# Kernel optimization log

Hardware: AMD Instinct MI355X
Metric: run time of the kernel (lower is better)

The kernel has to match this reference:

```python
import jax, jax.numpy as jnp
import numpy as np

B = 16      # number of point clouds in the batch
N = 2048    # points per cloud
P = B * N   # total points (flat PyG-style batching)
K = 16      # neighbors per point (col 0 = self loop)
OUT = 512   # out_channels


def _linear(key, fi, fo):
    # torch nn.Linear default init: U(-1/sqrt(fi), 1/sqrt(fi))
    s = 1.0 / np.sqrt(fi)
    kw, kb = jax.random.split(key)
    W = jax.random.uniform(kw, (fi, fo), jnp.float32, -s, s)
    b = jax.random.uniform(kb, (fo,), jnp.float32, -s, s)
    return W, b


def setup_inputs() -> dict:
    key = jax.random.key(0)
    ks = jax.random.split(key, 6)
    pos = jax.random.normal(ks[0], (P, 3), jnp.float32)
    # flat batch vector: points are grouped contiguously per cloud
    batch = (jnp.arange(P, dtype=jnp.int32) // N).astype(jnp.int32)
    # within-cloud random neighbor indices (stand-in for knn/radius graph)
    base = (jnp.arange(P) // N) * N  # offset of each point's cloud
    nbr = base[:, None] + jax.random.randint(ks[1], (P, K), 0, N)
    nbr = nbr.at[:, 0].set(jnp.arange(P))  # self loop (PyG add_self_loops)
    W1, b1 = _linear(ks[2], 3, 64)          # sa1 MLP layer 1
    W2, b2 = _linear(ks[3], 64, 128)        # sa1 MLP layer 2
    W3, b3 = _linear(ks[4], 128 + 3, 256)   # sa2 MLP layer 1
    W4, b4 = _linear(ks[5], 256, OUT)       # sa2 MLP layer 2
    return dict(pos=pos, nbr=nbr.astype(jnp.int64), batch=batch,
                W1=W1, b1=b1, W2=W2, b2=b2, W3=W3, b3=b3, W4=W4, b4=b4)


def reference(pos, nbr, batch, W1, b1, W2, b2, W3, b3, W4, b4):
    # ----- sa1: x is None -> message = MLP(pos_j - pos_i), max-aggregated -----
    diff = pos[nbr] - pos[:, None, :]                      # [P, K, 3]
    h1 = jnp.maximum(diff @ W1 + b1, 0.0) @ W2 + b2        # [P, K, 128]
    x1 = jnp.max(h1, axis=1)                               # [P, 128]
    # ----- sa2: message = MLP([x1_j, pos_j - pos_i]), max-aggregated -----
    feats = jnp.concatenate([x1[nbr], diff], axis=-1)      # [P, K, 131]
    h2 = jnp.maximum(feats @ W3 + b3, 0.0) @ W4 + b4       # [P, K, 512]
    x2 = jnp.max(h2, axis=1)                               # [P, 512]
    # ----- global_max_pool over batch -----
    return jax.ops.segment_max(x2, batch, num_segments=B)  # [B, 512]
```

## Files before the change

kernel.cpp:

```cpp
#include <hip/hip_runtime.h>
#include <hip/hip_bf16.h>

#define PTOT   32768
#define KNB    16
#define NCLOUD 16
#define OUTC   512
#define A1S    168
#define A2S    264

typedef __attribute__((ext_vector_type(8)))  short v8bf;
typedef __attribute__((ext_vector_type(16))) float v16f;

__device__ __forceinline__ unsigned short f2b(float v) {
    __hip_bfloat16 h = __float2bfloat16(v);
    return *reinterpret_cast<unsigned short*>(&h);
}
__device__ __forceinline__ unsigned pk2(float a, float b) {
    return (unsigned)f2b(a) | ((unsigned)f2b(b) << 16);
}
__device__ __forceinline__ unsigned fenc(float f) {
    unsigned u = __float_as_uint(f);
    return (u & 0x80000000u) ? ~u : (u | 0x80000000u);
}
__device__ __forceinline__ float fdec(unsigned u) {
    unsigned b = (u & 0x80000000u) ? (u & 0x7FFFFFFFu) : ~u;
    return __uint_as_float(b);
}
__device__ __forceinline__ v16f zero16() {
    v16f z;
    #pragma unroll
    for (int i = 0; i < 16; ++i) z[i] = 0.0f;
    return z;
}

__global__ __launch_bounds__(256) void sa1_kernel(
    const float* __restrict__ pos, const int* __restrict__ nbr,
    const float* __restrict__ W1, const float* __restrict__ b1,
    const float* __restrict__ W2, const float* __restrict__ b2,
    const float* __restrict__ W3, const float* __restrict__ W4,
    unsigned short* __restrict__ W3s, unsigned short* __restrict__ W4s,
    unsigned* __restrict__ encbuf,
    unsigned short* __restrict__ x1b)
{
    __shared__ unsigned short A1d[128 * 16];
    __shared__ unsigned short A2[128 * 72];
    const int tid  = threadIdx.x;
    const int lane = tid & 63;
    const int wave = tid >> 6;
    const int l31  = lane & 31;
    const int h    = lane >> 5;

    {
        int ip = blockIdx.x * 256 + tid;
        if (ip < 40960) {
            int j = ip & 7, n = (ip >> 3) & 255, c2 = ip >> 11;
            int k = c2 * 8 + j;
            W3s[ip] = f2b(k < 131 ? W3[k * 256 + n] : 0.0f);
        }
        int i2 = ip - 40960;
        if (i2 >= 0 && i2 < 131072) {
            int j = i2 & 7, n = (i2 >> 3) & 511, c2 = i2 >> 12;
            int k = c2 * 8 + j;
            W4s[i2] = f2b(W4[k * 512 + n]);
        }
        if (blockIdx.x == 4095) {
            for (int i = tid; i < NCLOUD * OUTC; i += 256) encbuf[i] = 0u;
        }
    }

    const int c1 = (wave >> 1) * 32 + l31;
    v8bf b1f;
    #pragma unroll
    for (int i = 0; i < 8; ++i) b1f[i] = 0;
    if (h == 0) {
        b1f[0] = (short)f2b(W1[c1]);
        b1f[1] = (short)f2b(W1[64 + c1]);
        b1f[2] = (short)f2b(W1[128 + c1]);
    }
    const float b1v = b1[c1];
    const int cW2 = wave * 32 + l31;
    v8bf B2[4];
    #pragma unroll
    for (int kc = 0; kc < 4; ++kc)
        #pragma unroll
        for (int j = 0; j < 8; ++j)
            B2[kc][j] = (short)f2b(W2[(kc * 16 + h * 8 + j) * 128 + cW2]);
    const float b2v = b2[cW2];

    const int p0 = blockIdx.x * 8;

    if (tid < 128) {
        int r = tid;
        int j = nbr[p0 * KNB + r];
        int p = p0 + (r >> 4);
        v8bf z;
        #pragma unroll
        for (int i = 0; i < 8; ++i) z[i] = 0;
        v8bf dv = z;
        dv[0] = (short)f2b(pos[j * 3 + 0] - pos[p * 3 + 0]);
        dv[1] = (short)f2b(pos[j * 3 + 1] - pos[p * 3 + 1]);
        dv[2] = (short)f2b(pos[j * 3 + 2] - pos[p * 3 + 2]);
        *(v8bf*)(A1d + r * 16)     = dv;
        *(v8bf*)(A1d + r * 16 + 8) = z;
    }
    __syncthreads();

    #pragma unroll
    for (int rr = 0; rr < 2; ++rr) {
        const int rt = (wave & 1) + rr * 2;
        v8bf a = *(const v8bf*)(A1d + (rt * 32 + l31) * 16 + h * 8);
        v16f acc = __builtin_amdgcn_mfma_f32_32x32x16_bf16(a, b1f, zero16(), 0, 0, 0);
        #pragma unroll
        for (int r = 0; r < 16; ++r) {
            int row = rt * 32 + (r & 3) + 8 * (r >> 2) + 4 * h;
            A2[row * 72 + c1] = f2b(fmaxf(acc[r] + b1v, 0.0f));
        }
    }
    __syncthreads();

    #pragma unroll
    for (int rt = 0; rt < 4; ++rt) {
        v16f acc = zero16();
        #pragma unroll
        for (int kc = 0; kc < 4; ++kc) {
            v8bf a = *(const v8bf*)(A2 + (rt * 32 + l31) * 72 + kc * 16 + h * 8);
            acc = __builtin_amdgcn_mfma_f32_32x32x16_bf16(a, B2[kc], acc, 0, 0, 0);
        }
        float ma = acc[0], mb = acc[8];
        #pragma unroll
        for (int r = 1; r < 8; ++r) { ma = fmaxf(ma, acc[r]); mb = fmaxf(mb, acc[8 + r]); }
        ma = fmaxf(ma, __shfl_xor(ma, 32));
        mb = fmaxf(mb, __shfl_xor(mb, 32));
        int p = p0 + rt * 2 + h;
        float m = h ? mb : ma;
        x1b[p * 128 + cW2] = f2b(m + b2v);
    }
}

__global__ __launch_bounds__(256) void sa2_kernel(
    const float* __restrict__ pos, const int* __restrict__ nbr,
    const int* __restrict__ batch,
    const unsigned short* __restrict__ W3s, const float* __restrict__ b3,
    const unsigned short* __restrict__ W4s, const float* __restrict__ b4,
    const unsigned short* __restrict__ x1b, unsigned* __restrict__ encbuf)
{
    __shared__ unsigned short S[128 * A2S];
    const int tid  = threadIdx.x;
    const int lane = tid & 63;
    const int wave = tid >> 6;
    const int l31  = lane & 31;
    const int h    = lane >> 5;
    const int p0   = blockIdx.x * 8;

    const float b3v0 = b3[(wave * 2 + 0) * 32 + l31];
    const float b3v1 = b3[(wave * 2 + 1) * 32 + l31];

    {
        int r = tid >> 1, q = tid & 1;
        int j = nbr[p0 * KNB + r];
        const uint4* src = (const uint4*)(x1b + j * 128 + q * 64);
        uint4* dst = (uint4*)(S + r * A1S + q * 64);
        #pragma unroll
        for (int i = 0; i < 8; ++i) dst[i] = src[i];
    }
    if (tid < 128) {
        int r = tid;
        int j = nbr[p0 * KNB + r];
        int p = p0 + (r >> 4);
        v8bf z;
        #pragma unroll
        for (int i = 0; i < 8; ++i) z[i] = 0;
        v8bf dv = z;
        dv[0] = (short)f2b(pos[j * 3 + 0] - pos[p * 3 + 0]);
        dv[1] = (short)f2b(pos[j * 3 + 1] - pos[p * 3 + 1]);
        dv[2] = (short)f2b(pos[j * 3 + 2] - pos[p * 3 + 2]);
        *(v8bf*)(S + r * A1S + 128) = dv;
        *(v8bf*)(S + r * A1S + 136) = z;
    }
    __syncthreads();

    const int n1a = (wave * 2 + 0) * 32 + l31;
    const int n1b = (wave * 2 + 1) * 32 + l31;
    unsigned stA[2][16], stB[2][16];
    #pragma unroll
    for (int rtp = 0; rtp < 2; ++rtp) {
        v16f g00 = zero16(), g01 = zero16(), g10 = zero16(), g11 = zero16();
        #pragma unroll
        for (int kc = 0; kc < 9; ++kc) {
            v8bf a0 = *(const v8bf*)(S + (rtp * 64 + l31)      * A1S + kc * 16 + h * 8);
            v8bf a1 = *(const v8bf*)(S + (rtp * 64 + 32 + l31) * A1S + kc * 16 + h * 8);
            int c2 = kc * 2 + h;
            v8bf B0 = *(const v8bf*)(W3s + ((c2 * 256 + n1a) << 3));
            v8bf B1 = *(const v8bf*)(W3s + ((c2 * 256 + n1b) << 3));
            g00 = __builtin_amdgcn_mfma_f32_32x32x16_bf16(a0, B0, g00, 0, 0, 0);
            g10 = __builtin_amdgcn_mfma_f32_32x32x16_bf16(a1, B0, g10, 0, 0, 0);
            g01 = __builtin_amdgcn_mfma_f32_32x32x16_bf16(a0, B1, g01, 0, 0, 0);
            g11 = __builtin_amdgcn_mfma_f32_32x32x16_bf16(a1, B1, g11, 0, 0, 0);
        }
        #pragma unroll
        for (int i = 0; i < 8; ++i) {
            stA[rtp][i]     = pk2(fmaxf(g00[2*i] + b3v0, 0.0f), fmaxf(g00[2*i+1] + b3v0, 0.0f));
            stA[rtp][8 + i] = pk2(fmaxf(g10[2*i] + b3v0, 0.0f), fmaxf(g10[2*i+1] + b3v0, 0.0f));
            stB[rtp][i]     = pk2(fmaxf(g01[2*i] + b3v1, 0.0f), fmaxf(g01[2*i+1] + b3v1, 0.0f));
            stB[rtp][8 + i] = pk2(fmaxf(g11[2*i] + b3v1, 0.0f), fmaxf(g11[2*i+1] + b3v1, 0.0f));
        }
    }
    __syncthreads();

    {
        const int c0 = (wave * 2 + 0) * 32 + l31;
        const int c1 = (wave * 2 + 1) * 32 + l31;
        #pragma unroll
        for (int rtp = 0; rtp < 2; ++rtp) {
            const int rb = rtp * 64;
            #pragma unroll
            for (int i = 0; i < 8; ++i) {
                int row = rb + ((2*i) & 3) + 8 * ((2*i) >> 2) + 4 * h;
                S[row * A2S + c0]        = (unsigned short)(stA[rtp][i] & 0xFFFF);
                S[(row + 1) * A2S + c0]  = (unsigned short)(stA[rtp][i] >> 16);
                S[(row + 32) * A2S + c0] = (unsigned short)(stA[rtp][8 + i] & 0xFFFF);
                S[(row + 33) * A2S + c0] = (unsigned short)(stA[rtp][8 + i] >> 16);
                S[row * A2S + c1]        = (unsigned short)(stB[rtp][i] & 0xFFFF);
                S[(row + 1) * A2S + c1]  = (unsigned short)(stB[rtp][i] >> 16);
                S[(row + 32) * A2S + c1] = (unsigned short)(stB[rtp][8 + i] & 0xFFFF);
                S[(row + 33) * A2S + c1] = (unsigned short)(stB[rtp][8 + i] >> 16);
            }
        }
    }
    __syncthreads();

    const int cloud = batch[p0];
    #pragma unroll
    for (int cp = 0; cp < 2; ++cp) {
        const int ct0 = wave * 4 + cp * 2;
        const int n0 = ct0 * 32 + l31;
        const int n1 = (ct0 + 1) * 32 + l31;
        v8bf B2a[16], B2b[16];
        #pragma unroll
        for (int kc = 0; kc < 16; ++kc) {
            int c2 = kc * 2 + h;
            B2a[kc] = *(const v8bf*)(W4s + ((c2 * 512 + n0) << 3));
            B2b[kc] = *(const v8bf*)(W4s + ((c2 * 512 + n1) << 3));
        }
        float rm0 = -3.4e38f, rm1 = -3.4e38f;
        #pragma unroll
        for (int rtp = 0; rtp < 2; ++rtp) {
            v16f a00 = zero16(), a01 = zero16(), a10 = zero16(), a11 = zero16();
            #pragma unroll
            for (int kc = 0; kc < 16; ++kc) {
                v8bf a0 = *(const v8bf*)(S + (rtp * 64 + l31)      * A2S + kc * 16 + h * 8);
                v8bf a1 = *(const v8bf*)(S + (rtp * 64 + 32 + l31) * A2S + kc * 16 + h * 8);
                a00 = __builtin_amdgcn_mfma_f32_32x32x16_bf16(a0, B2a[kc], a00, 0, 0, 0);
                a10 = __builtin_amdgcn_mfma_f32_32x32x16_bf16(a1, B2a[kc], a10, 0, 0, 0);
                a01 = __builtin_amdgcn_mfma_f32_32x32x16_bf16(a0, B2b[kc], a01, 0, 0, 0);
                a11 = __builtin_amdgcn_mfma_f32_32x32x16_bf16(a1, B2b[kc], a11, 0, 0, 0);
            }
            #pragma unroll
            for (int r = 0; r < 16; ++r) {
                rm0 = fmaxf(rm0, fmaxf(a00[r], a10[r]));
                rm1 = fmaxf(rm1, fmaxf(a01[r], a11[r]));
            }
        }
        rm0 = fmaxf(rm0, __shfl_xor(rm0, 32));
        rm1 = fmaxf(rm1, __shfl_xor(rm1, 32));
        rm0 += b4[ct0 * 32 + l31];
        rm1 += b4[(ct0 + 1) * 32 + l31];
        if (lane < 32) {
            atomicMax(&encbuf[cloud * OUTC + ct0 * 32 + l31], fenc(rm0));
            atomicMax(&encbuf[cloud * OUTC + (ct0 + 1) * 32 + l31], fenc(rm1));
        }
    }
}

__global__ void finalize_kernel(const unsigned* __restrict__ encv,
                                float* __restrict__ out)
{
    int i = blockIdx.x * 256 + threadIdx.x;
    if (i < NCLOUD * OUTC) out[i] = fdec(encv[i]);
}

extern "C" void kernel_launch(void* const* d_in, const int* in_sizes, int n_in,
                              void* d_out, int out_size, void* d_ws, size_t ws_size,
                              hipStream_t stream)
{
    const float* pos   = (const float*)d_in[0];
    const int*   nbr   = (const int*)  d_in[1];
    const int*   batch = (const int*)  d_in[2];
    const float* W1    = (const float*)d_in[3];
    const float* b1    = (const float*)d_in[4];
    const float* W2    = (const float*)d_in[5];
    const float* b2    = (const float*)d_in[6];
    const float* W3    = (const float*)d_in[7];
    const float* b3    = (const float*)d_in[8];
    const float* W4    = (const float*)d_in[9];
    const float* b4    = (const float*)d_in[10];

    unsigned short* x1b = (unsigned short*)d_ws;
    unsigned short* W3s = (unsigned short*)((char*)d_ws + 8388608);
    unsigned short* W4s = (unsigned short*)((char*)d_ws + 8470528);
    unsigned*    encbuf = (unsigned*)((char*)d_ws + 8732672);

    sa1_kernel<<<PTOT / 8, 256, 0, stream>>>(pos, nbr, W1, b1, W2, b2, W3, W4,
                                             W3s, W4s, encbuf, x1b);
    sa2_kernel<<<PTOT / 8, 256, 0, stream>>>(pos, nbr, batch, W3s, b3, W4s, b4,
                                             x1b, encbuf);
    finalize_kernel<<<(NCLOUD * OUTC + 255) / 256, 256, 0, stream>>>(encbuf, (float*)d_out);
}
```

Before: 249.2 us.

## Compute sa2 first layer transposed from registers with folded bias and permlane repack

The sa2 first-layer GEMM is restructured so each wave keeps its gathered neighbor features in registers and computes W3^T·X (weights as the A operand), removing the shared-memory staging of gathered features and one barrier. The b3 bias is folded into the packed W3 matrix as an extra row paired with a constant 1.0 input, which removes the per-element bias add. Hidden activations are repacked with permlane32_swap into a k-chunked shared layout that allows 16-byte vector stores instead of scalar 16-bit stores, and the second GEMM reads that layout. The cost is redundant W3 fragment loads from global memory, and the bias is now rounded to bf16.

```diff
diff --git a/kernel.cpp b/kernel.cpp
--- a/kernel.cpp
+++ b/kernel.cpp
@@ -5,11 +5,10 @@
 #define KNB    16
 #define NCLOUD 16
 #define OUTC   512
-#define A1S    168
-#define A2S    264
 
 typedef __attribute__((ext_vector_type(8)))  short v8bf;
 typedef __attribute__((ext_vector_type(16))) float v16f;
+typedef __attribute__((ext_vector_type(2)))  unsigned int v2u;
 
 __device__ __forceinline__ unsigned short f2b(float v) {
     __hip_bfloat16 h = __float2bfloat16(v);
@@ -37,7 +36,8 @@
     const float* __restrict__ pos, const int* __restrict__ nbr,
     const float* __restrict__ W1, const float* __restrict__ b1,
     const float* __restrict__ W2, const float* __restrict__ b2,
-    const float* __restrict__ W3, const float* __restrict__ W4,
+    const float* __restrict__ W3, const float* __restrict__ b3,
+    const float* __restrict__ W4,
     unsigned short* __restrict__ W3s, unsigned short* __restrict__ W4s,
     unsigned* __restrict__ encbuf,
     unsigned short* __restrict__ x1b)
@@ -55,7 +55,8 @@
         if (ip < 40960) {
             int j = ip & 7, n = (ip >> 3) & 255, c2 = ip >> 11;
             int k = c2 * 8 + j;
-            W3s[ip] = f2b(k < 131 ? W3[k * 256 + n] : 0.0f);
+            float v = (k < 131) ? W3[k * 256 + n] : (k == 131 ? b3[n] : 0.0f);
+            W3s[ip] = f2b(v);
         }
         int i2 = ip - 40960;
         if (i2 >= 0 && i2 < 131072) {
@@ -140,92 +141,58 @@
 __global__ __launch_bounds__(256) void sa2_kernel(
     const float* __restrict__ pos, const int* __restrict__ nbr,
     const int* __restrict__ batch,
-    const unsigned short* __restrict__ W3s, const float* __restrict__ b3,
+    const unsigned short* __restrict__ W3s,
     const unsigned short* __restrict__ W4s, const float* __restrict__ b4,
     const unsigned short* __restrict__ x1b, unsigned* __restrict__ encbuf)
 {
-    __shared__ unsigned short S[128 * A2S];
+    __shared__ unsigned short S[16 * 2048];
     const int tid  = threadIdx.x;
     const int lane = tid & 63;
     const int wave = tid >> 6;
     const int l31  = lane & 31;
     const int h    = lane >> 5;
     const int p0   = blockIdx.x * 8;
-
-    const float b3v0 = b3[(wave * 2 + 0) * 32 + l31];
-    const float b3v1 = b3[(wave * 2 + 1) * 32 + l31];
-
+    const int row  = wave * 32 + l31;
+
+    const int j = nbr[p0 * KNB + row];
+    v8bf xf[9];
+    #pragma unroll
+    for (int kc = 0; kc < 8; ++kc)
+        xf[kc] = *(const v8bf*)(x1b + j * 128 + kc * 16 + h * 8);
     {
-        int r = tid >> 1, q = tid & 1;
-        int j = nbr[p0 * KNB + r];
-        const uint4* src = (const uint4*)(x1b + j * 128 + q * 64);
-        uint4* dst = (uint4*)(S + r * A1S + q * 64);
-        #pragma unroll
-        for (int i = 0; i < 8; ++i) dst[i] = src[i];
-    }
-    if (tid < 128) {
-        int r = tid;
-        int j = nbr[p0 * KNB + r];
-        int p = p0 + (r >> 4);
         v8bf z;
         #pragma unroll
         for (int i = 0; i < 8; ++i) z[i] = 0;
-        v8bf dv = z;
-        dv[0] = (short)f2b(pos[j * 3 + 0] - pos[p * 3 + 0]);
-        dv[1] = (short)f2b(pos[j * 3 + 1] - pos[p * 3 + 1]);
-        dv[2] = (short)f2b(pos[j * 3 + 2] - pos[p * 3 + 2]);
-        *(v8bf*)(S + r * A1S + 128) = dv;
-        *(v8bf*)(S + r * A1S + 136) = z;
-    }
-    __syncthreads();
-
-    const int n1a = (wave * 2 + 0) * 32 + l31;
-    const int n1b = (wave * 2 + 1) * 32 + l31;
-    unsigned stA[2][16], stB[2][16];
-    #pragma unroll
-    for (int rtp = 0; rtp < 2; ++rtp) {
-        v16f g00 = zero16(), g01 = zero16(), g10 = zero16(), g11 = zero16();
+        if (h == 0) {
+            int p = p0 + (row >> 4);
+            z[0] = (short)f2b(pos[j * 3 + 0] - pos[p * 3 + 0]);
+            z[1] = (short)f2b(pos[j * 3 + 1] - pos[p * 3 + 1]);
+            z[2] = (short)f2b(pos[j * 3 + 2] - pos[p * 3 + 2]);
+            z[3] = (short)0x3F80;
+        }
+        xf[8] = z;
+    }
+
+    #pragma unroll
+    for (int ct = 0; ct < 8; ++ct) {
+        v16f acc = zero16();
         #pragma unroll
         for (int kc = 0; kc < 9; ++kc) {
-            v8bf a0 = *(const v8bf*)(S + (rtp * 64 + l31)      * A1S + kc * 16 + h * 8);
-            v8bf a1 = *(const v8bf*)(S + (rtp * 64 + 32 + l31) * A1S + kc * 16 + h * 8);
-            int c2 = kc * 2 + h;
-            v8bf B0 = *(const v8bf*)(W3s + ((c2 * 256 + n1a) << 3));
-            v8bf B1 = *(const v8bf*)(W3s + ((c2 * 256 + n1b) << 3));
-            g00 = __builtin_amdgcn_mfma_f32_32x32x16_bf16(a0, B0, g00, 0, 0, 0);
-            g10 = __builtin_amdgcn_mfma_f32_32x32x16_bf16(a1, B0, g10, 0, 0, 0);
-            g01 = __builtin_amdgcn_mfma_f32_32x32x16_bf16(a0, B1, g01, 0, 0, 0);
-            g11 = __builtin_amdgcn_mfma_f32_32x32x16_bf16(a1, B1, g11, 0, 0, 0);
-        }
-        #pragma unroll
-        for (int i = 0; i < 8; ++i) {
-            stA[rtp][i]     = pk2(fmaxf(g00[2*i] + b3v0, 0.0f), fmaxf(g00[2*i+1] + b3v0, 0.0f));
-            stA[rtp][8 + i] = pk2(fmaxf(g10[2*i] + b3v0, 0.0f), fmaxf(g10[2*i+1] + b3v0, 0.0f));
-            stB[rtp][i]     = pk2(fmaxf(g01[2*i] + b3v1, 0.0f), fmaxf(g01[2*i+1] + b3v1, 0.0f));
-            stB[rtp][8 + i] = pk2(fmaxf(g11[2*i] + b3v1, 0.0f), fmaxf(g11[2*i+1] + b3v1, 0.0f));
-        }
-    }
-    __syncthreads();
-
-    {
-        const int c0 = (wave * 2 + 0) * 32 + l31;
-        const int c1 = (wave * 2 + 1) * 32 + l31;
-        #pragma unroll
-        for (int rtp = 0; rtp < 2; ++rtp) {
-            const int rb = rtp * 64;
-            #pragma unroll
-            for (int i = 0; i < 8; ++i) {
-                int row = rb + ((2*i) & 3) + 8 * ((2*i) >> 2) + 4 * h;
-                S[row * A2S + c0]        = (unsigned short)(stA[rtp][i] & 0xFFFF);
-                S[(row + 1) * A2S + c0]  = (unsigned short)(stA[rtp][i] >> 16);
-                S[(row + 32) * A2S + c0] = (unsigned short)(stA[rtp][8 + i] & 0xFFFF);
-                S[(row + 33) * A2S + c0] = (unsigned short)(stA[rtp][8 + i] >> 16);
-                S[row * A2S + c1]        = (unsigned short)(stB[rtp][i] & 0xFFFF);
-                S[(row + 1) * A2S + c1]  = (unsigned short)(stB[rtp][i] >> 16);
-                S[(row + 32) * A2S + c1] = (unsigned short)(stB[rtp][8 + i] & 0xFFFF);
-                S[(row + 33) * A2S + c1] = (unsigned short)(stB[rtp][8 + i] >> 16);
-            }
-        }
+            const int c2 = kc * 2 + h;
+            v8bf wf = *(const v8bf*)(W3s + ((c2 * 256 + ct * 32 + l31) << 3));
+            acc = __builtin_amdgcn_mfma_f32_32x32x16_bf16(wf, xf[kc], acc, 0, 0, 0);
+        }
+        float m[16];
+        #pragma unroll
+        for (int r = 0; r < 16; ++r) m[r] = fmaxf(acc[r], 0.0f);
+        v2u s0 = __builtin_amdgcn_permlane32_swap(pk2(m[0],  m[1]),  pk2(m[4],  m[5]),  false, false);
+        v2u s1 = __builtin_amdgcn_permlane32_swap(pk2(m[2],  m[3]),  pk2(m[6],  m[7]),  false, false);
+        v2u s2 = __builtin_amdgcn_permlane32_swap(pk2(m[8],  m[9]),  pk2(m[12], m[13]), false, false);
+        v2u s3 = __builtin_amdgcn_permlane32_swap(pk2(m[10], m[11]), pk2(m[14], m[15]), false, false);
+        uint4 f0; f0.x = s0[0]; f0.y = s1[0]; f0.z = s0[1]; f0.w = s1[1];
+        uint4 f1; f1.x = s2[0]; f1.y = s3[0]; f1.z = s2[1]; f1.w = s3[1];
+        *reinterpret_cast<uint4*>(S + (2 * ct)     * 2048 + h * 1024 + row * 8) = f0;
+        *reinterpret_cast<uint4*>(S + (2 * ct + 1) * 2048 + h * 1024 + row * 8) = f1;
     }
     __syncthreads();
 
@@ -248,8 +215,8 @@
             v16f a00 = zero16(), a01 = zero16(), a10 = zero16(), a11 = zero16();
             #pragma unroll
             for (int kc = 0; kc < 16; ++kc) {
-                v8bf a0 = *(const v8bf*)(S + (rtp * 64 + l31)      * A2S + kc * 16 + h * 8);
-                v8bf a1 = *(const v8bf*)(S + (rtp * 64 + 32 + l31) * A2S + kc * 16 + h * 8);
+                v8bf a0 = *(const v8bf*)(S + kc * 2048 + h * 1024 + (rtp * 64 + l31) * 8);
+                v8bf a1 = *(const v8bf*)(S + kc * 2048 + h * 1024 + (rtp * 64 + 32 + l31) * 8);
                 a00 = __builtin_amdgcn_mfma_f32_32x32x16_bf16(a0, B2a[kc], a00, 0, 0, 0);
                 a10 = __builtin_amdgcn_mfma_f32_32x32x16_bf16(a1, B2a[kc], a10, 0, 0, 0);
                 a01 = __builtin_amdgcn_mfma_f32_32x32x16_bf16(a0, B2b[kc], a01, 0, 0, 0);
@@ -300,9 +267,9 @@
     unsigned short* W4s = (unsigned short*)((char*)d_ws + 8470528);
     unsigned*    encbuf = (unsigned*)((char*)d_ws + 8732672);
 
-    sa1_kernel<<<PTOT / 8, 256, 0, stream>>>(pos, nbr, W1, b1, W2, b2, W3, W4,
+    sa1_kernel<<<PTOT / 8, 256, 0, stream>>>(pos, nbr, W1, b1, W2, b2, W3, b3, W4,
                                              W3s, W4s, encbuf, x1b);
-    sa2_kernel<<<PTOT / 8, 256, 0, stream>>>(pos, nbr, batch, W3s, b3, W4s, b4,
+    sa2_kernel<<<PTOT / 8, 256, 0, stream>>>(pos, nbr, batch, W3s, W4s, b4,
                                              x1b, encbuf);
     finalize_kernel<<<(NCLOUD * OUTC + 255) / 256, 256, 0, stream>>>(encbuf, (float*)d_out);
 }
```

After: 287.6 us. +15.4%, slower.
